# Kernel tuning notes

Hardware: AMD Instinct MI355X
Metric: run time of the kernel (lower is better)

## Reference

```python
import jax, jax.numpy as jnp
import numpy as np
import math

D_MODEL = 1024
NUM_HEADS = 16
HEAD_DIM = D_MODEL // NUM_HEADS
EPS = 1e-6
ROPE_BASE = 10000.0


def _rope_cos_sin(seq_len, dim, dtype):
    inv_freq = 1.0 / (ROPE_BASE ** (jnp.arange(0, dim, 2, dtype=jnp.float32) / dim))
    t = jnp.arange(seq_len, dtype=jnp.float32)
    freqs = jnp.outer(t, inv_freq)                 # [s, dim/2]
    emb = jnp.concatenate([freqs, freqs], axis=-1)  # [s, dim]
    return jnp.cos(emb).astype(dtype), jnp.sin(emb).astype(dtype)


def _rotate_half(x):
    x1, x2 = jnp.split(x, 2, axis=-1)
    return jnp.concatenate([-x2, x1], axis=-1)


def setup_inputs() -> dict:
    key = jax.random.key(0)
    k1, k2, k3 = jax.random.split(key, 3)
    b, s = 2, 2048
    x = jax.random.normal(k1, (b, s, D_MODEL), dtype=jnp.float32)
    norm_w = jnp.ones((D_MODEL,), dtype=jnp.float32)
    qkv_w = jax.random.normal(k2, (3 * D_MODEL, D_MODEL), dtype=jnp.float32) * (1.0 / math.sqrt(D_MODEL))
    qkv_b = jnp.zeros((3 * D_MODEL,), dtype=jnp.float32)
    proj_w = jax.random.normal(k3, (D_MODEL, D_MODEL), dtype=jnp.float32) * (1.0 / math.sqrt(D_MODEL))
    proj_b = jnp.zeros((D_MODEL,), dtype=jnp.float32)
    return {"x": x, "norm_w": norm_w, "qkv_w": qkv_w, "qkv_b": qkv_b,
            "proj_w": proj_w, "proj_b": proj_b}


def reference(x, norm_w, qkv_w, qkv_b, proj_w, proj_b):
    b, s, d = x.shape
    # RMSNorm (pre-LN)
    xn = x * jax.lax.rsqrt(jnp.mean(x * x, axis=-1, keepdims=True) + EPS) * norm_w
    # Fused QKV
    qkv = jnp.einsum('bsd,ed->bse', xn, qkv_w) + qkv_b
    q, k, v = jnp.split(qkv, 3, axis=-1)
    # [b, h, s, hd]
    def shape(t):
        return t.reshape(b, s, NUM_HEADS, HEAD_DIM).transpose(0, 2, 1, 3)
    q, k, v = shape(q), shape(k), shape(v)
    # RoPE on head_dim
    cos, sin = _rope_cos_sin(s, HEAD_DIM, x.dtype)  # [s, hd]
    q = q * cos + _rotate_half(q) * sin
    k = k * cos + _rotate_half(k) * sin
    # Naive causal attention
    scale = 1.0 / math.sqrt(HEAD_DIM)
    scores = jnp.einsum('bhqd,bhkd->bhqk', q, k) * scale
    causal = jnp.tril(jnp.ones((s, s), dtype=bool))
    scores = jnp.where(causal, scores, -jnp.inf)
    attn = jax.nn.softmax(scores, axis=-1)
    y = jnp.einsum('bhqk,bhkd->bhqd', attn, v)
    y = y.transpose(0, 2, 1, 3).reshape(b, s, d)
    return jnp.einsum('bsd,ed->bse', y, proj_w) + proj_b
```

## Files before the change

### kernel.cpp

```cpp
#include <hip/hip_runtime.h>
#include <cstdint>
#include <cstddef>

#define NB 2
#define NS 2048
#define ND 1024
#define NH 16
#define HD 64
#define ROWS 4096
#define E3 3072

using bf16 = __bf16;
typedef __attribute__((ext_vector_type(4))) __bf16 bf16x4;
typedef __attribute__((ext_vector_type(8))) __bf16 bf16x8;
typedef __attribute__((ext_vector_type(4))) float f32x4;

__device__ __forceinline__ f32x4 mfma16(bf16x8 a, bf16x8 b, f32x4 c) {
    return __builtin_amdgcn_mfma_f32_16x16x32_bf16(a, b, c, 0, 0, 0);
}

__device__ __forceinline__ void gll16(const bf16* src, bf16* lds) {
    __builtin_amdgcn_global_load_lds(
        (const __attribute__((address_space(1))) void*)src,
        (__attribute__((address_space(3))) void*)lds, 16, 0, 0);
}

__global__ __launch_bounds__(256) void rope_table(float4* __restrict__ tab) {
    int idx = blockIdx.x * 256 + threadIdx.x;
    int s = idx >> 4, j = idx & 15;
    float f0 = powf(10000.0f, -(float)j * (1.0f / 32.0f));
    float f1 = powf(10000.0f, -(float)(j + 16) * (1.0f / 32.0f));
    float sn0, c0, sn1, c1;
    sincosf((float)s * f0, &sn0, &c0);
    sincosf((float)s * f1, &sn1, &c1);
    tab[idx] = make_float4(c0, sn0, c1, sn1);
}

__global__ __launch_bounds__(256) void cast_weights(const float* __restrict__ qkv_w,
                                                    const float* __restrict__ proj_w,
                                                    bf16* __restrict__ wq) {
    const int n1 = E3 * ND;
    int i = (blockIdx.x * 256 + threadIdx.x) * 4;
    const float* src = (i < n1) ? (qkv_w + i) : (proj_w + (i - n1));
    float4 v = *(const float4*)src;
    bf16x4 o;
    o[0] = (bf16)v.x; o[1] = (bf16)v.y; o[2] = (bf16)v.z; o[3] = (bf16)v.w;
    *(bf16x4*)(wq + i) = o;
}

__global__ __launch_bounds__(256) void rmsnorm_cast(const float* __restrict__ x,
                                                    const float* __restrict__ w,
                                                    bf16* __restrict__ xn) {
    int row = blockIdx.x;
    int tid = threadIdx.x;
    const float* xr = x + (size_t)row * ND;
    float4 v = ((const float4*)xr)[tid];
    float ss = v.x*v.x + v.y*v.y + v.z*v.z + v.w*v.w;
    #pragma unroll
    for (int m = 32; m >= 1; m >>= 1) ss += __shfl_xor(ss, m);
    __shared__ float wsum[4];
    if ((tid & 63) == 0) wsum[tid >> 6] = ss;
    __syncthreads();
    float total = wsum[0] + wsum[1] + wsum[2] + wsum[3];
    float scale = rsqrtf(total * (1.0f / ND) + 1e-6f);
    float4 wv = ((const float4*)w)[tid];
    bf16x4 o;
    o[0] = (bf16)(v.x * scale * wv.x);
    o[1] = (bf16)(v.y * scale * wv.y);
    o[2] = (bf16)(v.z * scale * wv.z);
    o[3] = (bf16)(v.w * scale * wv.w);
    ((bf16x4*)(xn + (size_t)row * ND))[tid] = o;
}

__global__ __launch_bounds__(256) void gemm_qkv_rope(const bf16* __restrict__ A,
                                                     const bf16* __restrict__ Bm,
                                                     const float* __restrict__ bias,
                                                     const float4* __restrict__ tab,
                                                     bf16* __restrict__ Qb,
                                                     bf16* __restrict__ Kb,
                                                     bf16* __restrict__ Vt) {
    const int K = ND;
    __shared__ bf16 Asm[128 * 32];
    __shared__ bf16 Bsm[128 * 32];
    const int tid = threadIdx.x;
    const int wave = tid >> 6, lane = tid & 63;
    const int quad = lane >> 4, l15 = lane & 15;
    const int row0 = blockIdx.x * 128, col0 = blockIdx.y * 128;
    const int wr = (wave >> 1) * 64, wc = (wave & 1) * 64;
    const int srow = lane >> 2;
    const int scol = (lane & 3) * 8;

    f32x4 acc[4][4] = {};

    for (int k0 = 0; k0 < K; k0 += 32) {
        #pragma unroll
        for (int i = 0; i < 2; ++i) {
            int r = wave * 32 + i * 16;
            gll16(A + (size_t)(row0 + r + srow) * K + k0 + scol, Asm + r * 32);
            gll16(Bm + (size_t)(col0 + r + srow) * K + k0 + scol, Bsm + r * 32);
        }
        __syncthreads();
        bf16x8 af[4], bff[4];
        #pragma unroll
        for (int t = 0; t < 4; ++t) {
            af[t]  = *(const bf16x8*)(Asm + (wr + t * 16 + l15) * 32 + quad * 8);
            bff[t] = *(const bf16x8*)(Bsm + (wc + t * 16 + l15) * 32 + quad * 8);
        }
        #pragma unroll
        for (int mt = 0; mt < 4; ++mt)
            #pragma unroll
            for (int nt = 0; nt < 4; ++nt)
                acc[mt][nt] = mfma16(af[mt], bff[nt], acc[mt][nt]);
        __syncthreads();
    }

    float bb[4];
    #pragma unroll
    for (int nt = 0; nt < 4; ++nt) bb[nt] = bias[col0 + wc + nt * 16 + l15];

    const int region = col0 >> 10;
    if (region == 2) {
        const int cv = col0 - 2048 + wc;
        const int h = cv >> 6;
        const int b = row0 >> 11;
        const int sloc = row0 & (NS - 1);
        #pragma unroll
        for (int nt = 0; nt < 4; ++nt) {
            const int d = nt * 16 + l15;
            bf16* vrow = Vt + ((size_t)(b * NH + h) * 64 + d) * NS;
            #pragma unroll
            for (int mt = 0; mt < 4; ++mt) {
                int sp = sloc + wr + (mt >> 1) * 32 + quad * 8 + (mt & 1) * 4;
                bf16x4 o4;
                #pragma unroll
                for (int r = 0; r < 4; ++r) o4[r] = (bf16)(acc[mt][nt][r] + bb[nt]);
                *(bf16x4*)(vrow + sp) = o4;
            }
        }
    } else {
        const float scale = (region == 0) ? 0.125f : 1.0f;
        bf16* Ob = (region == 0) ? Qb : Kb;
        const int h = ((col0 + wc) & 1023) >> 6;
        #pragma unroll
        for (int mt = 0; mt < 4; ++mt) {
            #pragma unroll
            for (int r = 0; r < 4; ++r) {
                int row = row0 + wr + mt * 16 + quad * 4 + r;
                int s = row & (NS - 1);
                int b = row >> 11;
                float4 cs = tab[s * 16 + l15];
                size_t obase = ((size_t)(b * NH + h) * NS + s) * 64;
                #pragma unroll
                for (int nt = 0; nt < 4; ++nt) {
                    float v  = acc[mt][nt][r] + bb[nt];
                    float vp = acc[mt][nt ^ 2][r] + bb[nt ^ 2];
                    float cc = (nt & 1) ? cs.z : cs.x;
                    float ss = (nt & 1) ? cs.w : cs.y;
                    float res = (nt < 2) ? (v * cc - vp * ss) : (v * cc + vp * ss);
                    Ob[obase + nt * 16 + l15] = (bf16)(res * scale);
                }
            }
        }
    }
}

__global__ __launch_bounds__(256) void gemm_bt_f32(const bf16* __restrict__ A,
                                                   const bf16* __restrict__ Bm,
                                                   const float* __restrict__ bias,
                                                   float* __restrict__ C,
                                                   int M, int N, int K) {
    __shared__ bf16 Asm[128 * 32];
    __shared__ bf16 Bsm[128 * 32];
    const int tid = threadIdx.x;
    const int wave = tid >> 6, lane = tid & 63;
    const int quad = lane >> 4, l15 = lane & 15;
    const int row0 = blockIdx.x * 128, col0 = blockIdx.y * 128;
    const int wr = (wave >> 1) * 64, wc = (wave & 1) * 64;
    const int srow = lane >> 2;
    const int scol = (lane & 3) * 8;

    f32x4 acc[4][4] = {};

    for (int k0 = 0; k0 < K; k0 += 32) {
        #pragma unroll
        for (int i = 0; i < 2; ++i) {
            int r = wave * 32 + i * 16;
            gll16(A + (size_t)(row0 + r + srow) * K + k0 + scol, Asm + r * 32);
            gll16(Bm + (size_t)(col0 + r + srow) * K + k0 + scol, Bsm + r * 32);
        }
        __syncthreads();
        bf16x8 af[4], bff[4];
        #pragma unroll
        for (int t = 0; t < 4; ++t) {
            af[t]  = *(const bf16x8*)(Asm + (wr + t * 16 + l15) * 32 + quad * 8);
            bff[t] = *(const bf16x8*)(Bsm + (wc + t * 16 + l15) * 32 + quad * 8);
        }
        #pragma unroll
        for (int mt = 0; mt < 4; ++mt)
            #pragma unroll
            for (int nt = 0; nt < 4; ++nt)
                acc[mt][nt] = mfma16(af[mt], bff[nt], acc[mt][nt]);
        __syncthreads();
    }

    #pragma unroll
    for (int nt = 0; nt < 4; ++nt) {
        int col = col0 + wc + nt * 16 + l15;
        float bv = bias[col];
        #pragma unroll
        for (int mt = 0; mt < 4; ++mt) {
            int row = row0 + wr + mt * 16 + quad * 4;
            #pragma unroll
            for (int r = 0; r < 4; ++r)
                C[(size_t)(row + r) * N + col] = acc[mt][nt][r] + bv;
        }
    }
}

__global__ __launch_bounds__(256) void attn(const bf16* __restrict__ Q,
                                            const bf16* __restrict__ K,
                                            const bf16* __restrict__ Vt,
                                            bf16* __restrict__ Y) {
    __shared__ bf16 Ksm[2][8192];
    __shared__ bf16 Vsm[2][8192];
    int bid = blockIdx.x;
    int g = bid >> 5;
    int bh = bid & 31;
    int qt = (g < 8) ? (15 - g) : (g - 8);
    int tid = threadIdx.x;
    int wave = tid >> 6, lane = tid & 63;
    int quad = lane >> 4, l15 = lane & 15;
    int q0 = qt * 128 + wave * 32;
    const bf16* Qh = Q + (size_t)bh * NS * 64;
    const bf16* Kh = K + (size_t)bh * NS * 64;
    const bf16* Vh = Vt + (size_t)bh * 64 * NS;
    const float NEG_INF = -__builtin_inff();

    const int krow = wave * 8 + (lane >> 3);
    const int ksx  = (lane & 7) ^ (krow & 7);
    const bf16* sK = Kh + (size_t)krow * 64 + ksx * 8;
    const int vrow = wave * 4 + (lane >> 4);
    const int vcx  = (lane & 15) ^ (vrow & 15);
    const bf16* sV = Vh + (size_t)vrow * NS + vcx * 8;

    const bf16* pk0 = &Ksm[0][l15 * 64 + ((quad) ^ (l15 & 7)) * 8];
    const bf16* pk1 = &Ksm[0][l15 * 64 + ((4 + quad) ^ (l15 & 7)) * 8];
    const bf16* pvk[4];
    #pragma unroll
    for (int ks = 0; ks < 4; ++ks)
        pvk[ks] = &Vsm[0][l15 * 128 + ((ks * 4 + quad) ^ l15) * 8];

    bf16x8 bq[2][2];
    #pragma unroll
    for (int t = 0; t < 2; ++t)
        #pragma unroll
        for (int hh = 0; hh < 2; ++hh)
            bq[t][hh] = *(const bf16x8*)(Qh + (size_t)(q0 + t * 16 + l15) * 64 + hh * 32 + quad * 8);

    f32x4 o[2][4] = {};
    float lsum[2] = {0.f, 0.f};

    auto stage = [&](int c, int par) {
        const int kb = c * 128;
        bf16* dK = &Ksm[par][wave * 512];
        bf16* dV = &Vsm[par][wave * 512];
        #pragma unroll
        for (int i = 0; i < 4; ++i)
            gll16(sK + (size_t)(kb + i * 32) * 64, dK + i * 2048);
        #pragma unroll
        for (int i = 0; i < 4; ++i)
            gll16(sV + kb + (size_t)(i * 16) * NS, dV + i * 2048);
    };

    auto compute = [&](int cc, int par) {
        const int kb = cc * 128;
        const int pb = par * 8192;
        #pragma unroll
        for (int ksub = 0; ksub < 4; ++ksub) {
            const int kbs = kb + ksub * 32;
            if (kbs <= q0) {
                bf16x8 ak00 = *(const bf16x8*)(pk0 + pb + ksub * 2048);
                bf16x8 ak01 = *(const bf16x8*)(pk1 + pb + ksub * 2048);
                bf16x8 ak10 = *(const bf16x8*)(pk0 + pb + ksub * 2048 + 1024);
                bf16x8 ak11 = *(const bf16x8*)(pk1 + pb + ksub * 2048 + 1024);
                bf16x8 vf0 = *(const bf16x8*)(pvk[ksub] + pb);
                bf16x8 vf1 = *(const bf16x8*)(pvk[ksub] + pb + 2048);
                bf16x8 vf2 = *(const bf16x8*)(pvk[ksub] + pb + 4096);
                bf16x8 vf3 = *(const bf16x8*)(pvk[ksub] + pb + 6144);
                const bool masked = (kbs == q0);
                #pragma unroll
                for (int t = 0; t < 2; ++t) {
                    f32x4 sh0 = {}, sh1 = {};
                    sh0 = mfma16(ak00, bq[t][0], sh0);
                    sh0 = mfma16(ak01, bq[t][1], sh0);
                    sh1 = mfma16(ak10, bq[t][0], sh1);
                    sh1 = mfma16(ak11, bq[t][1], sh1);
                    if (masked) {
                        int qy = q0 + t * 16 + l15;
                        #pragma unroll
                        for (int r = 0; r < 4; ++r) {
                            if (kbs + quad * 4 + r > qy)      sh0[r] = NEG_INF;
                            if (kbs + 16 + quad * 4 + r > qy) sh1[r] = NEG_INF;
                        }
                    }
                    bf16x8 pa;
                    float ls = 0.f;
                    #pragma unroll
                    for (int j = 0; j < 4; ++j) {
                        float p0 = __expf(sh0[j]);
                        float p1 = __expf(sh1[j]);
                        ls += p0 + p1;
                        pa[j] = (bf16)p0;
                        pa[4 + j] = (bf16)p1;
                    }
                    lsum[t] += ls;
                    o[t][0] = mfma16(pa, vf0, o[t][0]);
                    o[t][1] = mfma16(pa, vf1, o[t][1]);
                    o[t][2] = mfma16(pa, vf2, o[t][2]);
                    o[t][3] = mfma16(pa, vf3, o[t][3]);
                }
            }
        }
    };

    const int ncb = qt + 1;
    stage(0, 0);
    __syncthreads();
    for (int c = 0; c < ncb; ++c) {
        const int par = c & 1;
        if (c + 1 < ncb) stage(c + 1, par ^ 1);
        compute(c, par);
        __syncthreads();
    }

    int b = bh >> 4, h = bh & 15;
    #pragma unroll
    for (int t = 0; t < 2; ++t) {
        float red = lsum[t];
        red += __shfl_xor(red, 16);
        red += __shfl_xor(red, 32);
        #pragma unroll
        for (int r = 0; r < 4; ++r) {
            float il = 1.0f / __shfl(red, quad * 4 + r);
            size_t row = (size_t)(b * NS + q0 + t * 16 + quad * 4 + r);
            #pragma unroll
            for (int nt = 0; nt < 4; ++nt)
                Y[row * ND + h * 64 + nt * 16 + l15] = (bf16)(o[t][nt][r] * il);
        }
    }
}

extern "C" void kernel_launch(void* const* d_in, const int* in_sizes, int n_in,
                              void* d_out, int out_size, void* d_ws, size_t ws_size,
                              hipStream_t stream) {
    const float* x      = (const float*)d_in[0];
    const float* norm_w = (const float*)d_in[1];
    const float* qkv_w  = (const float*)d_in[2];
    const float* qkv_b  = (const float*)d_in[3];
    const float* proj_w = (const float*)d_in[4];
    const float* proj_b = (const float*)d_in[5];
    float* out = (float*)d_out;

    char* ws = (char*)d_ws;
    size_t off = 0;
    bf16* xn    = (bf16*)(ws + off); off += (size_t)ROWS * ND * 2;
    bf16* wq    = (bf16*)(ws + off); off += (size_t)E3 * ND * 2;
    bf16* wp    = (bf16*)(ws + off); off += (size_t)ND * ND * 2;
    bf16* Qb    = (bf16*)(ws + off); off += (size_t)NB * NH * NS * HD * 2;
    bf16* Kb    = (bf16*)(ws + off); off += (size_t)NB * NH * NS * HD * 2;
    bf16* Vt    = (bf16*)(ws + off); off += (size_t)NB * NH * HD * NS * 2;
    bf16* Y     = (bf16*)(ws + off); off += (size_t)ROWS * ND * 2;
    float4* tab = (float4*)(ws + off); off += (size_t)NS * 16 * sizeof(float4);

    rope_table<<<NS * 16 / 256, 256, 0, stream>>>(tab);
    cast_weights<<<(E3 * ND + ND * ND) / 1024, 256, 0, stream>>>(qkv_w, proj_w, wq);
    rmsnorm_cast<<<ROWS, 256, 0, stream>>>(x, norm_w, xn);
    gemm_qkv_rope<<<dim3(ROWS / 128, E3 / 128), 256, 0, stream>>>(xn, wq, qkv_b, tab, Qb, Kb, Vt);
    attn<<<NB * NH * (NS / 128), 256, 0, stream>>>(Qb, Kb, Vt, Y);
    gemm_bt_f32<<<dim3(ROWS / 128, ND / 128), 256, 0, stream>>>(Y, wp, proj_b, out, ROWS, ND, ND);
}
```

Before: 198.7 us.

## Store V in MFMA fragment order and narrow projection GEMM tiles

The QKV GEMM epilogue now writes V in a pre-swizzled fragment layout that matches the per-lane MFMA operand order. Attention can then stage V with contiguous 16-byte loads and read each fragment with one linear LDS read instead of XOR-swizzled transposed accesses. Separately, the output projection GEMM uses 128x64 tiles to double its block count (256 to 512 blocks) for better CU occupancy, at the cost of less reuse of A per block.

```diff
diff --git a/kernel.cpp b/kernel.cpp
--- a/kernel.cpp
+++ b/kernel.cpp
@@ -78,7 +78,7 @@
                                                      const float4* __restrict__ tab,
                                                      bf16* __restrict__ Qb,
                                                      bf16* __restrict__ Kb,
-                                                     bf16* __restrict__ Vt) {
+                                                     bf16* __restrict__ Vf) {
     const int K = ND;
     __shared__ bf16 Asm[128 * 32];
     __shared__ bf16 Bsm[128 * 32];
@@ -124,17 +124,19 @@
         const int h = cv >> 6;
         const int b = row0 >> 11;
         const int sloc = row0 & (NS - 1);
-        #pragma unroll
-        for (int nt = 0; nt < 4; ++nt) {
-            const int d = nt * 16 + l15;
-            bf16* vrow = Vt + ((size_t)(b * NH + h) * 64 + d) * NS;
-            #pragma unroll
-            for (int mt = 0; mt < 4; ++mt) {
-                int sp = sloc + wr + (mt >> 1) * 32 + quad * 8 + (mt & 1) * 4;
-                bf16x4 o4;
+        const int kg0 = (sloc + wr) >> 5;
+        bf16* vh = Vf + (size_t)(b * NH + h) * 131072;
+        #pragma unroll
+        for (int Gw = 0; Gw < 2; ++Gw) {
+            #pragma unroll
+            for (int nt = 0; nt < 4; ++nt) {
+                bf16x8 vf8;
                 #pragma unroll
-                for (int r = 0; r < 4; ++r) o4[r] = (bf16)(acc[mt][nt][r] + bb[nt]);
-                *(bf16x4*)(vrow + sp) = o4;
+                for (int r = 0; r < 4; ++r) {
+                    vf8[r]     = (bf16)(acc[2 * Gw][nt][r] + bb[nt]);
+                    vf8[4 + r] = (bf16)(acc[2 * Gw + 1][nt][r] + bb[nt]);
+                }
+                *(bf16x8*)(vh + ((size_t)(kg0 + Gw) * 4 + nt) * 512 + lane * 8) = vf8;
             }
         }
     } else {
@@ -164,47 +166,44 @@
     }
 }
 
-__global__ __launch_bounds__(256) void gemm_bt_f32(const bf16* __restrict__ A,
-                                                   const bf16* __restrict__ Bm,
-                                                   const float* __restrict__ bias,
-                                                   float* __restrict__ C,
-                                                   int M, int N, int K) {
+__global__ __launch_bounds__(256) void gemm_proj(const bf16* __restrict__ A,
+                                                 const bf16* __restrict__ Bm,
+                                                 const float* __restrict__ bias,
+                                                 float* __restrict__ C) {
     __shared__ bf16 Asm[128 * 32];
-    __shared__ bf16 Bsm[128 * 32];
+    __shared__ bf16 Bsm[64 * 32];
     const int tid = threadIdx.x;
     const int wave = tid >> 6, lane = tid & 63;
     const int quad = lane >> 4, l15 = lane & 15;
-    const int row0 = blockIdx.x * 128, col0 = blockIdx.y * 128;
-    const int wr = (wave >> 1) * 64, wc = (wave & 1) * 64;
+    const int row0 = blockIdx.x * 128, col0 = blockIdx.y * 64;
+    const int wr = (wave >> 1) * 64, wc = (wave & 1) * 32;
     const int srow = lane >> 2;
     const int scol = (lane & 3) * 8;
 
-    f32x4 acc[4][4] = {};
-
-    for (int k0 = 0; k0 < K; k0 += 32) {
-        #pragma unroll
-        for (int i = 0; i < 2; ++i) {
-            int r = wave * 32 + i * 16;
-            gll16(A + (size_t)(row0 + r + srow) * K + k0 + scol, Asm + r * 32);
-            gll16(Bm + (size_t)(col0 + r + srow) * K + k0 + scol, Bsm + r * 32);
-        }
-        __syncthreads();
-        bf16x8 af[4], bff[4];
-        #pragma unroll
-        for (int t = 0; t < 4; ++t) {
-            af[t]  = *(const bf16x8*)(Asm + (wr + t * 16 + l15) * 32 + quad * 8);
+    f32x4 acc[4][2] = {};
+
+    for (int k0 = 0; k0 < ND; k0 += 32) {
+        gll16(A + (size_t)(row0 + wave * 32 + srow) * ND + k0 + scol, Asm + (wave * 32) * 32);
+        gll16(A + (size_t)(row0 + wave * 32 + 16 + srow) * ND + k0 + scol, Asm + (wave * 32 + 16) * 32);
+        gll16(Bm + (size_t)(col0 + wave * 16 + srow) * ND + k0 + scol, Bsm + (wave * 16) * 32);
+        __syncthreads();
+        bf16x8 af[4], bff[2];
+        #pragma unroll
+        for (int t = 0; t < 4; ++t)
+            af[t] = *(const bf16x8*)(Asm + (wr + t * 16 + l15) * 32 + quad * 8);
+        #pragma unroll
+        for (int t = 0; t < 2; ++t)
             bff[t] = *(const bf16x8*)(Bsm + (wc + t * 16 + l15) * 32 + quad * 8);
-        }
         #pragma unroll
         for (int mt = 0; mt < 4; ++mt)
             #pragma unroll
-            for (int nt = 0; nt < 4; ++nt)
+            for (int nt = 0; nt < 2; ++nt)
                 acc[mt][nt] = mfma16(af[mt], bff[nt], acc[mt][nt]);
         __syncthreads();
     }
 
     #pragma unroll
-    for (int nt = 0; nt < 4; ++nt) {
+    for (int nt = 0; nt < 2; ++nt) {
         int col = col0 + wc + nt * 16 + l15;
         float bv = bias[col];
         #pragma unroll
@@ -212,14 +211,14 @@
             int row = row0 + wr + mt * 16 + quad * 4;
             #pragma unroll
             for (int r = 0; r < 4; ++r)
-                C[(size_t)(row + r) * N + col] = acc[mt][nt][r] + bv;
+                C[(size_t)(row + r) * ND + col] = acc[mt][nt][r] + bv;
         }
     }
 }
 
 __global__ __launch_bounds__(256) void attn(const bf16* __restrict__ Q,
                                             const bf16* __restrict__ K,
-                                            const bf16* __restrict__ Vt,
+                                            const bf16* __restrict__ Vf,
                                             bf16* __restrict__ Y) {
     __shared__ bf16 Ksm[2][8192];
     __shared__ bf16 Vsm[2][8192];
@@ -233,22 +232,16 @@
     int q0 = qt * 128 + wave * 32;
     const bf16* Qh = Q + (size_t)bh * NS * 64;
     const bf16* Kh = K + (size_t)bh * NS * 64;
-    const bf16* Vh = Vt + (size_t)bh * 64 * NS;
     const float NEG_INF = -__builtin_inff();
 
     const int krow = wave * 8 + (lane >> 3);
     const int ksx  = (lane & 7) ^ (krow & 7);
     const bf16* sK = Kh + (size_t)krow * 64 + ksx * 8;
-    const int vrow = wave * 4 + (lane >> 4);
-    const int vcx  = (lane & 15) ^ (vrow & 15);
-    const bf16* sV = Vh + (size_t)vrow * NS + vcx * 8;
+    const bf16* sV = Vf + (size_t)bh * 131072 + wave * 2048 + lane * 8;
 
     const bf16* pk0 = &Ksm[0][l15 * 64 + ((quad) ^ (l15 & 7)) * 8];
     const bf16* pk1 = &Ksm[0][l15 * 64 + ((4 + quad) ^ (l15 & 7)) * 8];
-    const bf16* pvk[4];
-    #pragma unroll
-    for (int ks = 0; ks < 4; ++ks)
-        pvk[ks] = &Vsm[0][l15 * 128 + ((ks * 4 + quad) ^ l15) * 8];
+    const bf16* pvf = &Vsm[0][lane * 8];
 
     bf16x8 bq[2][2];
     #pragma unroll
@@ -263,13 +256,13 @@
     auto stage = [&](int c, int par) {
         const int kb = c * 128;
         bf16* dK = &Ksm[par][wave * 512];
-        bf16* dV = &Vsm[par][wave * 512];
+        bf16* dV = &Vsm[par][wave * 2048];
         #pragma unroll
         for (int i = 0; i < 4; ++i)
             gll16(sK + (size_t)(kb + i * 32) * 64, dK + i * 2048);
         #pragma unroll
-        for (int i = 0; i < 4; ++i)
-            gll16(sV + kb + (size_t)(i * 16) * NS, dV + i * 2048);
+        for (int nt = 0; nt < 4; ++nt)
+            gll16(sV + (size_t)(kb >> 5) * 2048 + nt * 512, dV + nt * 512);
     };
 
     auto compute = [&](int cc, int par) {
@@ -283,10 +276,10 @@
                 bf16x8 ak01 = *(const bf16x8*)(pk1 + pb + ksub * 2048);
                 bf16x8 ak10 = *(const bf16x8*)(pk0 + pb + ksub * 2048 + 1024);
                 bf16x8 ak11 = *(const bf16x8*)(pk1 + pb + ksub * 2048 + 1024);
-                bf16x8 vf0 = *(const bf16x8*)(pvk[ksub] + pb);
-                bf16x8 vf1 = *(const bf16x8*)(pvk[ksub] + pb + 2048);
-                bf16x8 vf2 = *(const bf16x8*)(pvk[ksub] + pb + 4096);
-                bf16x8 vf3 = *(const bf16x8*)(pvk[ksub] + pb + 6144);
+                bf16x8 vf0 = *(const bf16x8*)(pvf + pb + ksub * 2048);
+                bf16x8 vf1 = *(const bf16x8*)(pvf + pb + ksub * 2048 + 512);
+                bf16x8 vf2 = *(const bf16x8*)(pvf + pb + ksub * 2048 + 1024);
+                bf16x8 vf3 = *(const bf16x8*)(pvf + pb + ksub * 2048 + 1536);
                 const bool masked = (kbs == q0);
                 #pragma unroll
                 for (int t = 0; t < 2; ++t) {
@@ -368,14 +361,14 @@
     bf16* wp    = (bf16*)(ws + off); off += (size_t)ND * ND * 2;
     bf16* Qb    = (bf16*)(ws + off); off += (size_t)NB * NH * NS * HD * 2;
     bf16* Kb    = (bf16*)(ws + off); off += (size_t)NB * NH * NS * HD * 2;
-    bf16* Vt    = (bf16*)(ws + off); off += (size_t)NB * NH * HD * NS * 2;
+    bf16* Vfrag = (bf16*)(ws + off); off += (size_t)NB * NH * HD * NS * 2;
     bf16* Y     = (bf16*)(ws + off); off += (size_t)ROWS * ND * 2;
     float4* tab = (float4*)(ws + off); off += (size_t)NS * 16 * sizeof(float4);
 
     rope_table<<<NS * 16 / 256, 256, 0, stream>>>(tab);
     cast_weights<<<(E3 * ND + ND * ND) / 1024, 256, 0, stream>>>(qkv_w, proj_w, wq);
     rmsnorm_cast<<<ROWS, 256, 0, stream>>>(x, norm_w, xn);
-    gemm_qkv_rope<<<dim3(ROWS / 128, E3 / 128), 256, 0, stream>>>(xn, wq, qkv_b, tab, Qb, Kb, Vt);
-    attn<<<NB * NH * (NS / 128), 256, 0, stream>>>(Qb, Kb, Vt, Y);
-    gemm_bt_f32<<<dim3(ROWS / 128, ND / 128), 256, 0, stream>>>(Y, wp, proj_b, out, ROWS, ND, ND);
-}
+    gemm_qkv_rope<<<dim3(ROWS / 128, E3 / 128), 256, 0, stream>>>(xn, wq, qkv_b, tab, Qb, Kb, Vfrag);
+    attn<<<NB * NH * (NS / 128), 256, 0, stream>>>(Qb, Kb, Vfrag, Y);
+    gemm_proj<<<dim3(ROWS / 128, ND / 64), 256, 0, stream>>>(Y, wp, proj_b, out);
+}
```

Result: faster. 191.4 us (-3.7%).
